# Kernel optimization log

Hardware: AMD Instinct MI355X
Metric: run time of the kernel (lower is better)

Reference implementation:

```python
import jax, jax.numpy as jnp
import numpy as np

N = 30000        # nodes
K = 32           # max_neighs (fixed degree)
D = 128          # in_dim == out_dim
EPS = 1e-5       # BatchNorm eps (torch default)
DN = ('NCHW', 'OIHW', 'NCHW')


def setup_inputs() -> dict:
    key = jax.random.key(0)
    ks = jax.random.split(key, 8)
    h = jax.random.normal(ks[0], (N, D), dtype=jnp.float32)
    neighbors = jax.random.randint(ks[1], (N, K), 0, N, dtype=jnp.int64)
    # learned params (xavier-ish scale)
    Wfc = jax.random.normal(ks[2], (D, D), dtype=jnp.float32) * (1.0 / np.sqrt(D))
    Wa = jax.random.normal(ks[3], (1, 2 * D), dtype=jnp.float32) * 0.05
    wr = jax.random.normal(ks[4], (1, 1, 2, D), dtype=jnp.float32) * 0.05  # convrow kernel (2, in_dim)
    br = jnp.zeros((1,), jnp.float32)
    gr = jnp.ones((1,), jnp.float32)
    betar = jnp.zeros((1,), jnp.float32)
    wc = jax.random.normal(ks[5], (1, 1, K, 1), dtype=jnp.float32) * 0.05  # convcol kernel (max_neighs, 1)
    bc = jnp.zeros((1,), jnp.float32)
    gc = jnp.ones((1,), jnp.float32)
    betac = jnp.zeros((1,), jnp.float32)
    return {"h": h, "Wfc": Wfc, "Wa": Wa, "wr": wr, "br": br, "gr": gr,
            "betar": betar, "wc": wc, "bc": bc, "gc": gc, "betac": betac,
            "neighbors": neighbors}


def _batchnorm(x, gamma, beta):
    # training-mode BatchNorm2d: batch stats over (N, H, W), biased variance
    mean = jnp.mean(x, axis=(0, 2, 3), keepdims=True)
    var = jnp.var(x, axis=(0, 2, 3), keepdims=True)
    g = gamma.reshape(1, -1, 1, 1)
    b = beta.reshape(1, -1, 1, 1)
    return g * (x - mean) * jax.lax.rsqrt(var + EPS) + b


def reference(h, Wfc, Wa, wr, br, gr, betar, wc, bc, gc, betac, neighbors):
    z = h @ Wfc.T                                   # [N, D]
    z_src = z[neighbors]                            # [N, K, D] gather of src features
    a_src, a_dst = Wa[0, :D], Wa[0, D:]             # split attn weights (concat-linear)
    e = jax.nn.leaky_relu(z_src @ a_src + (z @ a_dst)[:, None])  # [N, K]
    alpha = jax.nn.softmax(e, axis=1)               # segment softmax over mailbox
    m = (alpha[..., None] * z_src)[:, None]         # [N, 1, K, D] weighted mailbox
    row = jax.lax.conv_general_dilated(m, wr, (1, 1), 'VALID', dimension_numbers=DN)
    row = jax.nn.relu(_batchnorm(row + br.reshape(1, -1, 1, 1), gr, betar))  # [N,1,K-1,1]
    col = jax.lax.conv_general_dilated(m, wc, (1, 1), 'VALID', dimension_numbers=DN)
    col = jax.nn.relu(_batchnorm(col + bc.reshape(1, -1, 1, 1), gc, betac))  # [N,1,1,D]
    n = m.shape[0]
    return jnp.concatenate([row.reshape(n, -1), col.reshape(n, -1)], axis=1)  # [N, K-1+D]
```

## Files before the change

kernel.cpp:

```cpp
#include <hip/hip_runtime.h>
#include <hip/hip_fp16.h>

#define NN 30000
#define DD 128
#define KK 32
#define OUTW 159
#define K2BLKS 1875
#define K3BLKS 1024

typedef __attribute__((ext_vector_type(8))) short bf16x8;
typedef __attribute__((ext_vector_type(4))) float f32x4;

static __device__ inline short f2bf(float f) {
  union { float f; unsigned u; } x; x.f = f;
  unsigned r = x.u + 0x7fffu + ((x.u >> 16) & 1u);
  return (short)(r >> 16);
}

__global__ __launch_bounds__(256) void k1_gemm(
    const float* __restrict__ h, const float* __restrict__ W,
    const float* __restrict__ Wa, const float* __restrict__ wr,
    __half* __restrict__ z, float* __restrict__ s, float* __restrict__ dv,
    float* __restrict__ zr0, float* __restrict__ zr1) {
  __shared__ char smem[48 * 1024];
  short* As = (short*)smem;
  short* Bs = (short*)(smem + 16 * 1024);
  const int tid = threadIdx.x;
  const int row0 = blockIdx.x * 64;

#pragma unroll
  for (int q = 0; q < 4; q++) {
    int idx = q * 256 + tid;
    int r = idx >> 4, kq = idx & 15;
    int row = row0 + r;
    float v[8];
    if (row < NN) {
      float4 v0 = *(const float4*)(h + (long)row * DD + kq * 8);
      float4 v1 = *(const float4*)(h + (long)row * DD + kq * 8 + 4);
      v[0]=v0.x; v[1]=v0.y; v[2]=v0.z; v[3]=v0.w;
      v[4]=v1.x; v[5]=v1.y; v[6]=v1.z; v[7]=v1.w;
    } else {
#pragma unroll
      for (int j = 0; j < 8; j++) v[j] = 0.f;
    }
    bf16x8 b;
#pragma unroll
    for (int j = 0; j < 8; j++) b[j] = f2bf(v[j]);
    *(bf16x8*)((char*)As + r * 256 + ((kq * 16) ^ ((r & 7) << 4))) = b;
  }
#pragma unroll
  for (int q = 0; q < 8; q++) {
    int idx = q * 256 + tid;
    int j0 = idx >> 4, kq = idx & 15;
    float4 v0 = *(const float4*)(W + (long)j0 * DD + kq * 8);
    float4 v1 = *(const float4*)(W + (long)j0 * DD + kq * 8 + 4);
    float v[8] = {v0.x, v0.y, v0.z, v0.w, v1.x, v1.y, v1.z, v1.w};
    bf16x8 b;
#pragma unroll
    for (int jj = 0; jj < 8; jj++) b[jj] = f2bf(v[jj]);
    *(bf16x8*)((char*)Bs + j0 * 256 + ((kq * 16) ^ ((j0 & 7) << 4))) = b;
  }
  __syncthreads();

  const int wid = tid >> 6, lane = tid & 63;
  const int la = lane & 15, lb = lane >> 4;

  bf16x8 afr[4];
#pragma unroll
  for (int kc = 0; kc < 4; kc++) {
    int r = wid * 16 + la;
    int cb2 = (kc * 32 + lb * 8) * 2;
    afr[kc] = *(bf16x8*)((char*)As + r * 256 + (cb2 ^ ((la & 7) << 4)));
  }

  f32x4 acc[8];
#pragma unroll
  for (int cb = 0; cb < 8; cb++) acc[cb] = (f32x4){0.f, 0.f, 0.f, 0.f};

#pragma unroll
  for (int cb = 0; cb < 8; cb++) {
    int j = cb * 16 + la;
#pragma unroll
    for (int kc = 0; kc < 4; kc++) {
      int cb2 = (kc * 32 + lb * 8) * 2;
      bf16x8 bfr = *(bf16x8*)((char*)Bs + j * 256 + (cb2 ^ ((la & 7) << 4)));
      acc[cb] = __builtin_amdgcn_mfma_f32_16x16x32_bf16(afr[kc], bfr, acc[cb], 0, 0, 0);
    }
  }

  float sa[4] = {0,0,0,0}, da[4] = {0,0,0,0}, r0s[4] = {0,0,0,0}, r1s[4] = {0,0,0,0};
#pragma unroll
  for (int cb = 0; cb < 8; cb++) {
    int c = cb * 16 + la;
    float wa0 = Wa[c], wa1 = Wa[DD + c], w0 = wr[c], w1 = wr[DD + c];
#pragma unroll
    for (int rg = 0; rg < 4; rg++) {
      float zv = acc[cb][rg];
      sa[rg]  += zv * wa0; da[rg]  += zv * wa1;
      r0s[rg] += zv * w0;  r1s[rg] += zv * w1;
    }
  }
#pragma unroll
  for (int rg = 0; rg < 4; rg++) {
#pragma unroll
    for (int o = 1; o < 16; o <<= 1) {
      sa[rg]  += __shfl_xor(sa[rg], o);
      da[rg]  += __shfl_xor(da[rg], o);
      r0s[rg] += __shfl_xor(r0s[rg], o);
      r1s[rg] += __shfl_xor(r1s[rg], o);
    }
    int row = row0 + wid * 16 + lb * 4 + rg;
    if (la == 0 && row < NN) {
      s[row] = sa[rg]; dv[row] = da[rg]; zr0[row] = r0s[rg]; zr1[row] = r1s[rg];
    }
  }

  __syncthreads();
  __half* zl = (__half*)smem;
#pragma unroll
  for (int cb = 0; cb < 8; cb++) {
#pragma unroll
    for (int rg = 0; rg < 4; rg++) {
      int r = wid * 16 + lb * 4 + rg, c = cb * 16 + la;
      zl[r * 132 + c] = __float2half(acc[cb][rg]);
    }
  }
  __syncthreads();
  {
    int r = tid >> 2, c0 = (tid & 3) * 32;
    int row = row0 + r;
    if (row < NN) {
      const __half* src = zl + r * 132 + c0;
      int4 a0 = *(const int4*)(src);
      int4 a1 = *(const int4*)(src + 8);
      int4 a2 = *(const int4*)(src + 16);
      int4 a3 = *(const int4*)(src + 24);
      __half* dst = z + (long)row * DD + c0;
      *(int4*)(dst)      = a0;
      *(int4*)(dst + 8)  = a1;
      *(int4*)(dst + 16) = a2;
      *(int4*)(dst + 24) = a3;
    }
  }
}

__global__ __launch_bounds__(256) void k2_main(
    const __half* __restrict__ z, const float* __restrict__ s,
    const float* __restrict__ dv, const float* __restrict__ zr0,
    const float* __restrict__ zr1, const int* __restrict__ nbr,
    const float* __restrict__ wc, const float* __restrict__ brp,
    const float* __restrict__ bcp,
    float* __restrict__ out, float* __restrict__ partials) {
  __shared__ float red[4][4];
  const int w = threadIdx.x >> 6, lane = threadIdx.x & 63;
  const int p = lane >> 4, m = lane & 15;
  const float br0 = brp[0], bc0 = bcp[0];
  float pr = 0.f, pr2 = 0.f, pc = 0.f, pc2 = 0.f;

#pragma unroll
  for (int it = 0; it < 4; it++) {
    int i = blockIdx.x * 16 + w * 4 + it;
    float dvi = dv[i];
    float aw = 0.f; int base = 0;
    if (lane < KK) {
      int nk = nbr[i * KK + lane];
      float e = s[nk] + dvi;
      e = e > 0.f ? e : 0.01f * e;
      float mx = e;
#pragma unroll
      for (int o = 16; o; o >>= 1) mx = fmaxf(mx, __shfl_xor(mx, o, 32));
      float ex = __expf(e - mx);
      float sm = ex;
#pragma unroll
      for (int o = 16; o; o >>= 1) sm += __shfl_xor(sm, o, 32);
      float alpha = ex / sm;

      float t1 = alpha * zr1[nk];
      float t1n = __shfl_down(t1, 1, 32);
      if (lane < KK - 1) {
        float v = alpha * zr0[nk] + t1n + br0;
        out[(long)i * OUTW + lane] = v;
        pr += v; pr2 += v * v;
      }
      aw = alpha * wc[lane];
      base = nk * DD;
    }

    float ac[8];
#pragma unroll
    for (int e = 0; e < 8; e++) ac[e] = 0.f;
#pragma unroll
    for (int t = 0; t < 8; t++) {
      int k = 4 * t + p;
      float a = __shfl(aw, k);
      int off = __shfl(base, k);
      int4 raw = *(const int4*)(z + off + m * 8);
      const __half2* hp = (const __half2*)&raw;
      float2 f0 = __half22float2(hp[0]);
      float2 f1 = __half22float2(hp[1]);
      float2 f2 = __half22float2(hp[2]);
      float2 f3 = __half22float2(hp[3]);
      ac[0] += a * f0.x; ac[1] += a * f0.y;
      ac[2] += a * f1.x; ac[3] += a * f1.y;
      ac[4] += a * f2.x; ac[5] += a * f2.y;
      ac[6] += a * f3.x; ac[7] += a * f3.y;
    }
#pragma unroll
    for (int e = 0; e < 8; e++) {
      ac[e] += __shfl_xor(ac[e], 16);
      ac[e] += __shfl_xor(ac[e], 32);
      ac[e] += bc0;
    }
    if (p == 0) {
      long ob = (long)i * OUTW + 31 + m * 8;
#pragma unroll
      for (int e = 0; e < 8; e++) {
        out[ob + e] = ac[e];
        pc += ac[e]; pc2 += ac[e] * ac[e];
      }
    }
  }

#pragma unroll
  for (int o = 32; o; o >>= 1) {
    pr  += __shfl_xor(pr, o);  pr2 += __shfl_xor(pr2, o);
    pc  += __shfl_xor(pc, o);  pc2 += __shfl_xor(pc2, o);
  }
  if (lane == 0) { red[w][0] = pr; red[w][1] = pr2; red[w][2] = pc; red[w][3] = pc2; }
  __syncthreads();
  if (threadIdx.x < 4) {
    float v = red[0][threadIdx.x] + red[1][threadIdx.x] +
              red[2][threadIdx.x] + red[3][threadIdx.x];
    partials[(long)blockIdx.x * 4 + threadIdx.x] = v;
  }
}

__global__ __launch_bounds__(256) void k3_fused(
    float* __restrict__ out, const float* __restrict__ partials,
    const float* __restrict__ gr, const float* __restrict__ betar,
    const float* __restrict__ gc, const float* __restrict__ betac) {
  __shared__ float red[4][4];
  __shared__ float coefs[4];
  const int w = threadIdx.x >> 6, lane = threadIdx.x & 63;

  float v0 = 0.f, v1 = 0.f, v2 = 0.f, v3 = 0.f;
  for (int idx = threadIdx.x; idx < K2BLKS; idx += 256) {
    float4 p = ((const float4*)partials)[idx];
    v0 += p.x; v1 += p.y; v2 += p.z; v3 += p.w;
  }
#pragma unroll
  for (int o = 32; o; o >>= 1) {
    v0 += __shfl_xor(v0, o); v1 += __shfl_xor(v1, o);
    v2 += __shfl_xor(v2, o); v3 += __shfl_xor(v3, o);
  }
  if (lane == 0) { red[w][0] = v0; red[w][1] = v1; red[w][2] = v2; red[w][3] = v3; }
  __syncthreads();
  if (threadIdx.x == 0) {
    float sr  = red[0][0] + red[1][0] + red[2][0] + red[3][0];
    float sr2 = red[0][1] + red[1][1] + red[2][1] + red[3][1];
    float sc  = red[0][2] + red[1][2] + red[2][2] + red[3][2];
    float sc2 = red[0][3] + red[1][3] + red[2][3] + red[3][3];
    const float cntR = (float)NN * 31.0f, cntC = (float)NN * 128.0f;
    float mR = sr / cntR,  vR = sr2 / cntR - mR * mR;
    float mC = sc / cntC,  vC = sc2 / cntC - mC * mC;
    float scR = gr[0] * rsqrtf(vR + 1e-5f);
    float scC = gc[0] * rsqrtf(vC + 1e-5f);
    coefs[0] = scR; coefs[1] = betar[0] - mR * scR;
    coefs[2] = scC; coefs[3] = betac[0] - mC * scC;
  }
  __syncthreads();
  const float scR = coefs[0], shR = coefs[1], scC = coefs[2], shC = coefs[3];

  const int TOT4 = NN * OUTW / 4;
  float4* o4 = (float4*)out;
  for (int f = blockIdx.x * 256 + threadIdx.x; f < TOT4; f += K3BLKS * 256) {
    float4 x = o4[f];
    int j = (4 * f) % OUTW;
    float r[4] = {x.x, x.y, x.z, x.w};
#pragma unroll
    for (int e = 0; e < 4; e++) {
      bool isRow = j < 31;
      r[e] = fmaxf((isRow ? scR : scC) * r[e] + (isRow ? shR : shC), 0.f);
      j = (j == OUTW - 1) ? 0 : j + 1;
    }
    o4[f] = make_float4(r[0], r[1], r[2], r[3]);
  }
}

extern "C" void kernel_launch(void* const* d_in, const int* in_sizes, int n_in,
                              void* d_out, int out_size, void* d_ws, size_t ws_size,
                              hipStream_t stream) {
  const float* h     = (const float*)d_in[0];
  const float* Wfc   = (const float*)d_in[1];
  const float* Wa    = (const float*)d_in[2];
  const float* wr    = (const float*)d_in[3];
  const float* br    = (const float*)d_in[4];
  const float* gr    = (const float*)d_in[5];
  const float* betar = (const float*)d_in[6];
  const float* wc    = (const float*)d_in[7];
  const float* bc    = (const float*)d_in[8];
  const float* gc    = (const float*)d_in[9];
  const float* betac = (const float*)d_in[10];
  const int*   nbr   = (const int*)d_in[11];
  float* out = (float*)d_out;

  float* ws   = (float*)d_ws;
  __half* z   = (__half*)ws;
  float* s    = ws + (long)NN * DD / 2;
  float* dv   = s  + NN;
  float* zr0  = dv + NN;
  float* zr1  = zr0 + NN;
  float* partials = zr1 + NN;

  k1_gemm<<<(NN + 63) / 64, 256, 0, stream>>>(h, Wfc, Wa, wr, z, s, dv, zr0, zr1);
  k2_main<<<K2BLKS, 256, 0, stream>>>(z, s, dv, zr0, zr1, nbr, wc, br, bc, out, partials);
  k3_fused<<<K3BLKS, 256, 0, stream>>>(out, partials, gr, betar, gc, betac);
}
```

Before: 60.59 us.

## Split attention and gather aggregation into separate kernels with two dimension passes

The fused main kernel is split into one kernel that computes the softmax attention, row-conv outputs and a packed (alpha*wc, neighbor offset) buffer, plus two gather kernels that each aggregate half of the feature dimension. Halving the gathered width per pass is meant to improve cache locality of the random z gathers, and nontemporal loads and stores keep streaming data out of cache. The cost is an extra intermediate buffer of N*K 64-bit entries written and read back, two more kernel launches, and a wider shuffle reduction in the gather kernels.

```diff
diff --git a/kernel.cpp b/kernel.cpp
--- a/kernel.cpp
+++ b/kernel.cpp
@@ -5,7 +5,9 @@
 #define DD 128
 #define KK 32
 #define OUTW 159
-#define K2BLKS 1875
+#define NA 938
+#define GP 1875
+#define NTOT (NA + 2 * GP)
 #define K3BLKS 1024
 
 typedef __attribute__((ext_vector_type(8))) short bf16x8;
@@ -144,57 +146,96 @@
   }
 }
 
-__global__ __launch_bounds__(256) void k2_main(
-    const __half* __restrict__ z, const float* __restrict__ s,
-    const float* __restrict__ dv, const float* __restrict__ zr0,
-    const float* __restrict__ zr1, const int* __restrict__ nbr,
-    const float* __restrict__ wc, const float* __restrict__ brp,
+__global__ __launch_bounds__(256) void k2a(
+    const float* __restrict__ s, const float* __restrict__ dv,
+    const float* __restrict__ zr0, const float* __restrict__ zr1,
+    const int* __restrict__ nbr, const float* __restrict__ wc,
+    const float* __restrict__ brp,
+    float* __restrict__ out, unsigned long long* __restrict__ awb,
+    float* __restrict__ partials) {
+  __shared__ float red[4][2];
+  const int w = threadIdx.x >> 6, lane = threadIdx.x & 63;
+  const int half = lane >> 5, kl = lane & 31;
+  const float br0 = brp[0];
+  const float wck = wc[kl];
+  float pr = 0.f, pr2 = 0.f;
+
+#pragma unroll
+  for (int it = 0; it < 4; it++) {
+    int i = blockIdx.x * 32 + w * 8 + it * 2 + half;
+    bool valid = i < NN;
+    int ii = valid ? i : 0;
+    float dvi = dv[ii];
+    int nk = __builtin_nontemporal_load(&nbr[ii * KK + kl]);
+    float e = s[nk] + dvi;
+    e = e > 0.f ? e : 0.01f * e;
+    float mx = e;
+#pragma unroll
+    for (int o = 16; o; o >>= 1) mx = fmaxf(mx, __shfl_xor(mx, o, 32));
+    float ex = __expf(e - mx);
+    float sm = ex;
+#pragma unroll
+    for (int o = 16; o; o >>= 1) sm += __shfl_xor(sm, o, 32);
+    float alpha = ex / sm;
+
+    float t1 = alpha * zr1[nk];
+    float t1n = __shfl_down(t1, 1, 32);
+    if (valid && kl < KK - 1) {
+      float v = alpha * zr0[nk] + t1n + br0;
+      __builtin_nontemporal_store(v, &out[(long)i * OUTW + kl]);
+      pr += v; pr2 += v * v;
+    }
+    if (valid) {
+      unsigned long long pk =
+          ((unsigned long long)(unsigned)(nk * DD) << 32) |
+          (unsigned long long)(unsigned)__float_as_int(alpha * wck);
+      __builtin_nontemporal_store(pk, &awb[i * KK + kl]);
+    }
+  }
+
+#pragma unroll
+  for (int o = 32; o; o >>= 1) {
+    pr += __shfl_xor(pr, o);  pr2 += __shfl_xor(pr2, o);
+  }
+  if (lane == 0) { red[w][0] = pr; red[w][1] = pr2; }
+  __syncthreads();
+  if (threadIdx.x == 0) {
+    float4 v = make_float4(red[0][0] + red[1][0] + red[2][0] + red[3][0],
+                           red[0][1] + red[1][1] + red[2][1] + red[3][1],
+                           0.f, 0.f);
+    ((float4*)partials)[blockIdx.x] = v;
+  }
+}
+
+__global__ __launch_bounds__(256) void k2p(
+    const __half* __restrict__ z, const unsigned long long* __restrict__ awb,
     const float* __restrict__ bcp,
-    float* __restrict__ out, float* __restrict__ partials) {
-  __shared__ float red[4][4];
+    float* __restrict__ out, float* __restrict__ partials, int pass, int pofs) {
+  __shared__ float red[4][2];
   const int w = threadIdx.x >> 6, lane = threadIdx.x & 63;
-  const int p = lane >> 4, m = lane & 15;
-  const float br0 = brp[0], bc0 = bcp[0];
-  float pr = 0.f, pr2 = 0.f, pc = 0.f, pc2 = 0.f;
+  const int p = lane >> 3, m = lane & 7;
+  const float bc0 = bcp[0];
+  const int dimbase = pass * 64;
+  float pc = 0.f, pc2 = 0.f;
 
 #pragma unroll
   for (int it = 0; it < 4; it++) {
     int i = blockIdx.x * 16 + w * 4 + it;
-    float dvi = dv[i];
     float aw = 0.f; int base = 0;
     if (lane < KK) {
-      int nk = nbr[i * KK + lane];
-      float e = s[nk] + dvi;
-      e = e > 0.f ? e : 0.01f * e;
-      float mx = e;
-#pragma unroll
-      for (int o = 16; o; o >>= 1) mx = fmaxf(mx, __shfl_xor(mx, o, 32));
-      float ex = __expf(e - mx);
-      float sm = ex;
-#pragma unroll
-      for (int o = 16; o; o >>= 1) sm += __shfl_xor(sm, o, 32);
-      float alpha = ex / sm;
-
-      float t1 = alpha * zr1[nk];
-      float t1n = __shfl_down(t1, 1, 32);
-      if (lane < KK - 1) {
-        float v = alpha * zr0[nk] + t1n + br0;
-        out[(long)i * OUTW + lane] = v;
-        pr += v; pr2 += v * v;
-      }
-      aw = alpha * wc[lane];
-      base = nk * DD;
-    }
-
+      unsigned long long pk = __builtin_nontemporal_load(&awb[i * KK + lane]);
+      aw = __int_as_float((int)(unsigned)pk);
+      base = (int)(pk >> 32);
+    }
     float ac[8];
 #pragma unroll
     for (int e = 0; e < 8; e++) ac[e] = 0.f;
 #pragma unroll
-    for (int t = 0; t < 8; t++) {
-      int k = 4 * t + p;
+    for (int t = 0; t < 4; t++) {
+      int k = 8 * t + p;
       float a = __shfl(aw, k);
       int off = __shfl(base, k);
-      int4 raw = *(const int4*)(z + off + m * 8);
+      int4 raw = *(const int4*)(z + off + dimbase + m * 8);
       const __half2* hp = (const __half2*)&raw;
       float2 f0 = __half22float2(hp[0]);
       float2 f1 = __half22float2(hp[1]);
@@ -207,15 +248,16 @@
     }
 #pragma unroll
     for (int e = 0; e < 8; e++) {
+      ac[e] += __shfl_xor(ac[e], 8);
       ac[e] += __shfl_xor(ac[e], 16);
       ac[e] += __shfl_xor(ac[e], 32);
       ac[e] += bc0;
     }
     if (p == 0) {
-      long ob = (long)i * OUTW + 31 + m * 8;
+      long ob = (long)i * OUTW + 31 + dimbase + m * 8;
 #pragma unroll
       for (int e = 0; e < 8; e++) {
-        out[ob + e] = ac[e];
+        __builtin_nontemporal_store(ac[e], &out[ob + e]);
         pc += ac[e]; pc2 += ac[e] * ac[e];
       }
     }
@@ -223,15 +265,15 @@
 
 #pragma unroll
   for (int o = 32; o; o >>= 1) {
-    pr  += __shfl_xor(pr, o);  pr2 += __shfl_xor(pr2, o);
-    pc  += __shfl_xor(pc, o);  pc2 += __shfl_xor(pc2, o);
-  }
-  if (lane == 0) { red[w][0] = pr; red[w][1] = pr2; red[w][2] = pc; red[w][3] = pc2; }
-  __syncthreads();
-  if (threadIdx.x < 4) {
-    float v = red[0][threadIdx.x] + red[1][threadIdx.x] +
-              red[2][threadIdx.x] + red[3][threadIdx.x];
-    partials[(long)blockIdx.x * 4 + threadIdx.x] = v;
+    pc += __shfl_xor(pc, o);  pc2 += __shfl_xor(pc2, o);
+  }
+  if (lane == 0) { red[w][0] = pc; red[w][1] = pc2; }
+  __syncthreads();
+  if (threadIdx.x == 0) {
+    float4 v = make_float4(0.f, 0.f,
+                           red[0][0] + red[1][0] + red[2][0] + red[3][0],
+                           red[0][1] + red[1][1] + red[2][1] + red[3][1]);
+    ((float4*)partials)[pofs + blockIdx.x] = v;
   }
 }
 
@@ -244,7 +286,7 @@
   const int w = threadIdx.x >> 6, lane = threadIdx.x & 63;
 
   float v0 = 0.f, v1 = 0.f, v2 = 0.f, v3 = 0.f;
-  for (int idx = threadIdx.x; idx < K2BLKS; idx += 256) {
+  for (int idx = threadIdx.x; idx < NTOT; idx += 256) {
     float4 p = ((const float4*)partials)[idx];
     v0 += p.x; v1 += p.y; v2 += p.z; v3 += p.w;
   }
@@ -306,13 +348,16 @@
 
   float* ws   = (float*)d_ws;
   __half* z   = (__half*)ws;
-  float* s    = ws + (long)NN * DD / 2;
+  float* s    = ws + (long)NN * 64;
   float* dv   = s  + NN;
   float* zr0  = dv + NN;
   float* zr1  = zr0 + NN;
-  float* partials = zr1 + NN;
+  unsigned long long* awb = (unsigned long long*)(zr1 + NN);
+  float* partials = (float*)(awb + (long)NN * KK);
 
   k1_gemm<<<(NN + 63) / 64, 256, 0, stream>>>(h, Wfc, Wa, wr, z, s, dv, zr0, zr1);
-  k2_main<<<K2BLKS, 256, 0, stream>>>(z, s, dv, zr0, zr1, nbr, wc, br, bc, out, partials);
+  k2a<<<NA, 256, 0, stream>>>(s, dv, zr0, zr1, nbr, wc, br, out, awb, partials);
+  k2p<<<GP, 256, 0, stream>>>(z, awb, bc, out, partials, 0, NA);
+  k2p<<<GP, 256, 0, stream>>>(z, awb, bc, out, partials, 1, NA + GP);
   k3_fused<<<K3BLKS, 256, 0, stream>>>(out, partials, gr, betar, gc, betac);
 }
```

Result: slower. 82.96 us (+36.9%).
